# Performance work log

Hardware: AMD Instinct MI355X
Metric: run time of the kernel (lower is better)

Reference implementation:

```python
import jax, jax.numpy as jnp
import numpy as np

LMAX, MMAX = 4, 2
C_IN, C_OUT = 128, 128           # sphere_channels, m_output_channels
NUM_EXPERTS = 8
NUM_SYSTEMS = 16
NUM_EDGES = 12288
M_SIZE = [LMAX + 1, 2 * (LMAX - 1 + 1), 2 * (LMAX - 2 + 1)]  # [5, 8, 6]


def _mole_linear(x, W, ce, b=None):
    """MoLE linear: per-edge expert mixing of weights, equivalently mixing of
    per-expert outputs.  x: [N, in] or [N, 2, in]; W: [K, in, out]; ce: [N, K]."""
    if x.ndim == 2:
        z = jnp.einsum('ni,kio->nko', x, W)        # [N, K, out]
        y = jnp.einsum('nk,nko->no', ce, z)
    else:
        z = jnp.einsum('nci,kio->nkco', x, W)      # [N, K, 2, out]
        y = jnp.einsum('nk,nkco->nco', ce, z)
    if b is not None:
        y = y + ce @ b                              # mixed bias, b: [K, out]
    return y


def setup_inputs() -> dict:
    key = jax.random.key(0)
    ks = jax.random.split(key, 8)
    num_mcoef = sum(M_SIZE)  # 19
    x = jax.random.normal(ks[0], (NUM_EDGES, num_mcoef, C_IN), dtype=jnp.float32)
    x_edge = jax.random.normal(ks[1], (NUM_EDGES, C_IN), dtype=jnp.float32)
    expert_coefficients = jax.random.uniform(ks[2], (NUM_SYSTEMS, NUM_EXPERTS), dtype=jnp.float32)
    edge_batch = jax.random.randint(ks[3], (NUM_EDGES,), 0, NUM_SYSTEMS)
    # fc_m0: in = (lmax+1)*C, out = (lmax+1)*C_out, with bias
    in0 = (LMAX + 1) * C_IN
    out0 = (LMAX + 1) * C_OUT
    W_m0 = jax.random.normal(ks[4], (NUM_EXPERTS, in0, out0), dtype=jnp.float32) * 0.02
    b_m0 = jnp.zeros((NUM_EXPERTS, out0), dtype=jnp.float32)
    # so2_m_conv m: in = (lmax-m+1)*C, out = 2*(lmax-m+1)*C_out, no bias
    nc1 = LMAX - 1 + 1
    W_m1 = jax.random.normal(ks[5], (NUM_EXPERTS, nc1 * C_IN, 2 * nc1 * C_OUT), dtype=jnp.float32) * 0.02
    nc2 = LMAX - 2 + 1
    W_m2 = jax.random.normal(ks[6], (NUM_EXPERTS, nc2 * C_IN, 2 * nc2 * C_OUT), dtype=jnp.float32) * 0.02
    return {
        'x': x, 'x_edge': x_edge,
        'expert_coefficients': expert_coefficients, 'edge_batch': edge_batch,
        'W_m0': W_m0, 'b_m0': b_m0, 'W_m1': W_m1, 'W_m2': W_m2,
    }


def reference(x, x_edge, expert_coefficients, edge_batch, W_m0, b_m0, W_m1, W_m2):
    N = x.shape[0]
    ce = expert_coefficients[edge_batch]               # [N, K] per-edge mix coeffs
    x0, x1, x2 = jnp.split(x, np.cumsum(M_SIZE[:-1]), axis=1)
    # m = 0 branch (internal_weights=True -> no radial rescale)
    y0 = _mole_linear(x0.reshape(N, -1), W_m0, ce, b_m0)
    out = [y0.reshape(N, -1, C_OUT)]                   # [N, lmax+1, C_out]
    # m >= 1 branches: SO(2) real/imag recombination
    for m, Wm, xm in ((1, W_m1, x1), (2, W_m2, x2)):
        nc = LMAX - m + 1
        xm = xm.reshape(N, 2, nc * C_IN)
        ym = _mole_linear(xm, Wm, ce)                  # [N, 2, 2*nc*C_out]
        ym = ym.reshape(N, 4, nc * C_OUT)
        x_m_r = ym[:, 0] - ym[:, 3]                    # x_r_0 - x_i_1
        x_m_i = ym[:, 2] + ym[:, 1]                    # x_r_1 + x_i_0
        out.append(x_m_r.reshape(N, nc, C_OUT))
        out.append(x_m_i.reshape(N, nc, C_OUT))
    return jnp.concatenate(out, axis=1)                # [N, 19, C_out]
```

## Files before the change

### kernel.cpp

```cpp
#include <hip/hip_runtime.h>
#include <cstdint>

#define N_EDGES 12288
#define ROWLEN  2432
#define CAP     2048

typedef __bf16 bf16;
typedef __bf16 bf16x8 __attribute__((ext_vector_type(8)));
typedef __bf16 bf16x4 __attribute__((ext_vector_type(4)));
typedef float  f32x4  __attribute__((ext_vector_type(4)));

#define SYS0 (640*640   + 2048)
#define SYS1 (1024*1024 + 2048)
#define SYS2 (768*768   + 2048)

#define WS_IDX_OFF   1024
#define WS_BIAS_OFF  (WS_IDX_OFF + 16*CAP*4)
#define WS_W_OFF     (WS_BIAS_OFF + 16*640*4)

template<int B> struct Cfg;
template<> struct Cfg<0> { static constexpr int K=640,  KS=640, XOFF=0,    NT=5;
                           static constexpr size_t SYS=SYS0, WOFF=0; };
template<> struct Cfg<1> { static constexpr int K=1024, KS=512, XOFF=640,  NT=8;
                           static constexpr size_t SYS=SYS1, WOFF=(size_t)16*SYS0; };
template<> struct Cfg<2> { static constexpr int K=768,  KS=384, XOFF=1664, NT=6;
                           static constexpr size_t SYS=SYS2,
                           WOFF=(size_t)16*SYS0+(size_t)16*SYS1; };

__device__ __forceinline__ void async_copy16(const void* g, void* l) {
  auto gp = reinterpret_cast<const __attribute__((address_space(1))) unsigned int*>(
      reinterpret_cast<uintptr_t>(g));
  auto lp = reinterpret_cast<__attribute__((address_space(3))) unsigned int*>(
      (unsigned int)reinterpret_cast<uintptr_t>(l));
  __builtin_amdgcn_global_load_lds(gp, lp, 16, 0, 0);
}

template<int B>
__device__ __forceinline__ void mix_body(const float* __restrict__ Wsrc,
                                         const float* ce_s,
                                         unsigned short* __restrict__ Wz,
                                         int pos, int estart) {
  constexpr int N = Cfg<B>::K, KS = Cfg<B>::KS, NT = N / 128, HALF = N / 2;
  constexpr int SRC_STRIDE = KS * N;
  constexpr size_t DST_STRIDE = Cfg<B>::SYS;
  int nn = pos & 127, kgrp = (pos >> 7) & 3, rest = pos >> 9;
  int nt = rest % NT, kblk = rest / NT;
  int i0 = kblk * 32 + kgrp * 8;
  int c  = nt * 128 + nn;
  int si = i0, sc = c; float sg = 1.f;
  if (B > 0 && i0 >= KS) {
    si = i0 - KS;
    if (c < HALF) { sc = c + HALF; sg = -1.f; } else { sc = c - HALF; }
  }
  unsigned short* db = Wz + Cfg<B>::WOFF + (size_t)pos * 8;
  const float* p0 = Wsrc + (size_t)si * N + sc;
#pragma unroll 1
  for (int jh = 0; jh < 2; ++jh) {
    float w[8][4];
#pragma unroll
    for (int t = 0; t < 8; ++t) {
      int ee = (t + estart) & 7;
      const float* p = p0 + (size_t)ee * SRC_STRIDE + (size_t)(jh * 4) * N;
#pragma unroll
      for (int j = 0; j < 4; ++j) w[t][j] = sg * p[(size_t)j * N];
    }
#pragma unroll
    for (int s = 0; s < 16; ++s) {
      float a[4] = {0, 0, 0, 0};
#pragma unroll
      for (int t = 0; t < 8; ++t) {
        float cc = ce_s[s * 8 + ((t + estart) & 7)];
#pragma unroll
        for (int j = 0; j < 4; ++j) a[j] += cc * w[t][j];
      }
      bf16x4 v;
      v[0] = (bf16)a[0]; v[1] = (bf16)a[1]; v[2] = (bf16)a[2]; v[3] = (bf16)a[3];
      *(bf16x4*)(db + s * DST_STRIDE + jh * 4) = v;
    }
  }
}

__global__ __launch_bounds__(256) void prep_all(
    const float* __restrict__ W0, const float* __restrict__ W1,
    const float* __restrict__ W2, const float* __restrict__ ce,
    unsigned short* __restrict__ Wz,
    const int* __restrict__ eb, int* __restrict__ counts, int* __restrict__ idxb,
    const float* __restrict__ b0, float* __restrict__ bias) {
  __shared__ float ce_s[128];
  __shared__ int hcnt[16], hbase[16];
  int tid = threadIdx.x;
  int bx = blockIdx.x;
  if (bx < 1000) {
    if (tid < 128) ce_s[tid] = ce[tid];
    __syncthreads();
    int estart = bx & 7;
    if (bx < 200)      mix_body<0>(W0, ce_s, Wz, bx * 256 + tid, estart);
    else if (bx < 712) mix_body<1>(W1, ce_s, Wz, (bx - 200) * 256 + tid, estart);
    else               mix_body<2>(W2, ce_s, Wz, (bx - 712) * 256 + tid, estart);
  } else if (bx < 1048) {
    int t = (bx - 1000) * 256 + tid;
    if (tid < 16) hcnt[tid] = 0;
    __syncthreads();
    int s = -1, lp = 0;
    if (t < N_EDGES) { s = eb[t]; lp = atomicAdd(&hcnt[s], 1); }
    __syncthreads();
    if (tid < 16) hbase[tid] = atomicAdd(counts + tid * 16, hcnt[tid]);
    __syncthreads();
    if (s >= 0) { int p = hbase[s] + lp; if (p < CAP) idxb[s * CAP + p] = t; }
  } else {
    int t = (bx - 1048) * 256 + tid;
    int s = t / 640, c = t - s * 640;
    float a = 0.f;
#pragma unroll
    for (int e = 0; e < 8; ++e) a += ce[s * 8 + e] * b0[e * 640 + c];
    bias[t] = a;
  }
}

template<int B>
__device__ __forceinline__ void gemm_body(
    const float* __restrict__ x,
    const unsigned short* __restrict__ Wz,
    const int* __restrict__ counts, const int* __restrict__ idxb,
    const float* __restrict__ bias, float* __restrict__ out,
    int s, int mt, int nt2, char* sm, int* eidx)
{
  constexpr int K = Cfg<B>::K, NT = Cfg<B>::NT, KB = K / 32, XOFF = Cfg<B>::XOFF;
  int cnt = counts[s * 16];
  int m0 = mt * 128;
  if (m0 >= cnt) return;
  int tid = threadIdx.x;
  if (tid < 128) eidx[tid] = (m0 + tid < cnt) ? idxb[s * CAP + m0 + tid] : -1;
  __syncthreads();
  char* Acur = sm;          char* Anxt = sm + 8192;
  char* Bc = sm + 16384;    char* Bm = sm + 32768;    char* Bn = sm + 49152;
  int wv = tid >> 6, ln = tid & 63;
  int wm = wv >> 2, wn = wv & 3;
  int kq = ln >> 4, lm = ln & 15;
  int c0 = nt2 * 2;
  int c16 = tid & 7, rbase = tid >> 3;
  int kq_w = c16 >> 1, half = c16 & 1;
  const char* xb = (const char*)x;
  unsigned int aoff[2], kinc[2];
#pragma unroll
  for (int i = 0; i < 2; ++i) {
    int e = eidx[rbase + 64 * i];
    aoff[i] = (e >= 0) ? (unsigned int)(((size_t)e * ROWLEN + XOFF) * 4) : 0u;
    kinc[i] = (e >= 0) ? 128u : 0u;
  }
  const unsigned short* wb = Wz + Cfg<B>::WOFF + (size_t)s * Cfg<B>::SYS;

  f32x4 sreg[2];
  auto loadA = [&](int kb) __attribute__((always_inline)) {
#pragma unroll
    for (int i = 0; i < 2; ++i)
      sreg[i] = *(const f32x4*)(xb + aoff[i] + kb * kinc[i] + c16 * 16);
  };
  auto writeA = [&](char* dst) __attribute__((always_inline)) {
#pragma unroll
    for (int i = 0; i < 2; ++i) {
      int r = rbase + 64 * i;
      bf16x4 v;
      v[0] = (bf16)sreg[i][0]; v[1] = (bf16)sreg[i][1];
      v[2] = (bf16)sreg[i][2]; v[3] = (bf16)sreg[i][3];
      *(bf16x4*)(dst + kq_w * 2048 + ((r ^ (kq_w << 1)) * 16) + half * 8) = v;
    }
  };
  auto stageB = [&](int kb, char* dst) __attribute__((always_inline)) {
    const unsigned short* base = wb + (size_t)kb * (NT * 4096);
#pragma unroll
    for (int i = 0; i < 2; ++i) {
      int c = i * 512 + tid;
      int ck = c0 + (c >> 9); if (ck > NT - 1) ck = NT - 1;
      async_copy16(base + (size_t)ck * 4096 + (c & 511) * 8,
                   dst + (i * 512 + wv * 64) * 16);
    }
  };

  f32x4 acc[4][4];
#pragma unroll
  for (int i = 0; i < 4; ++i)
#pragma unroll
    for (int j = 0; j < 4; ++j) {
      acc[i][j][0] = 0.f; acc[i][j][1] = 0.f; acc[i][j][2] = 0.f; acc[i][j][3] = 0.f;
    }

  stageB(0, Bc);
  loadA(0);
  writeA(Acur);
  stageB(1, Bm);
  loadA(1);
  asm volatile("s_waitcnt lgkmcnt(0)" ::: "memory");
  __builtin_amdgcn_s_barrier();
  __builtin_amdgcn_sched_barrier(0);

#pragma unroll 1
  for (int kb = 0; kb < KB; ++kb) {
    if (kb + 2 < KB) stageB(kb + 2, Bn);
    __builtin_amdgcn_sched_barrier(0);
    bf16x8 af[4], bq[4];
#pragma unroll
    for (int mi = 0; mi < 4; ++mi) {
      int r = wm * 64 + mi * 16 + lm;
      af[mi] = *(const bf16x8*)(Acur + kq * 2048 + ((r ^ (kq << 1)) * 16));
    }
#pragma unroll
    for (int ni = 0; ni < 4; ++ni)
      bq[ni] = *(const bf16x8*)(Bc + (wn >> 1) * 8192 + kq * 2048 +
                                (((wn & 1) * 64 + ni * 16 + lm) * 16));
    __builtin_amdgcn_s_setprio(1);
#pragma unroll
    for (int mi = 0; mi < 4; ++mi)
#pragma unroll
      for (int ni = 0; ni < 4; ++ni)
        acc[mi][ni] = __builtin_amdgcn_mfma_f32_16x16x32_bf16(af[mi], bq[ni], acc[mi][ni], 0, 0, 0);
    __builtin_amdgcn_s_setprio(0);
    if (kb + 1 < KB) {
      writeA(Anxt);
      if (kb + 2 < KB) loadA(kb + 2);
    }
    asm volatile("s_waitcnt lgkmcnt(0)" ::: "memory");
    __builtin_amdgcn_s_barrier();
    __builtin_amdgcn_sched_barrier(0);
    { char* t = Acur; Acur = Anxt; Anxt = t; }
    { char* tb = Bc; Bc = Bm; Bm = Bn; Bn = tb; }
  }
  int cc = c0 + (wn >> 1);
  if (cc >= NT) return;
  int colb = cc * 128 + (wn & 1) * 64;
  float bv[4] = {0, 0, 0, 0};
  if (B == 0) {
#pragma unroll
    for (int ni = 0; ni < 4; ++ni)
      bv[ni] = bias[s * 640 + colb + ni * 16 + lm];
  }
#pragma unroll
  for (int mi = 0; mi < 4; ++mi) {
#pragma unroll
    for (int r = 0; r < 4; ++r) {
      int row = wm * 64 + mi * 16 + kq * 4 + r;
      int e = eidx[row];
      if (e < 0) continue;
      float* po = out + (size_t)e * ROWLEN + XOFF + colb + lm;
#pragma unroll
      for (int ni = 0; ni < 4; ++ni) po[ni * 16] = acc[mi][ni][r] + bv[ni];
    }
  }
}

__global__ __launch_bounds__(512, 4) void gemm_all(
    const float* __restrict__ x,
    const unsigned short* __restrict__ Wz,
    const int* __restrict__ counts, const int* __restrict__ idxb,
    const float* __restrict__ bias, float* __restrict__ out) {
  extern __shared__ char sm[];
  __shared__ int eidx[128];
  int g = blockIdx.x;
  int xcd = g & 7, j = g >> 3;
  int s = xcd + 8 * (j / 160);
  int r = j % 160;
  int mt = r / 10, bx = r % 10;
  if (bx < 3)      gemm_body<0>(x, Wz, counts, idxb, bias, out, s, mt, bx,     sm, eidx);
  else if (bx < 7) gemm_body<1>(x, Wz, counts, idxb, bias, out, s, mt, bx - 3, sm, eidx);
  else             gemm_body<2>(x, Wz, counts, idxb, bias, out, s, mt, bx - 7, sm, eidx);
}

extern "C" void kernel_launch(void* const* d_in, const int* in_sizes, int n_in,
                              void* d_out, int out_size, void* d_ws, size_t ws_size,
                              hipStream_t stream) {
  const float* x  = (const float*)d_in[0];
  const float* ce = (const float*)d_in[2];
  const int*   eb = (const int*)d_in[3];
  const float* W0 = (const float*)d_in[4];
  const float* b0 = (const float*)d_in[5];
  const float* W1 = (const float*)d_in[6];
  const float* W2 = (const float*)d_in[7];
  float* out = (float*)d_out;
  char* ws = (char*)d_ws;
  int*   counts = (int*)ws;
  int*   idxb   = (int*)(ws + WS_IDX_OFF);
  float* bias   = (float*)(ws + WS_BIAS_OFF);
  unsigned short* Wz = (unsigned short*)(ws + WS_W_OFF);

  hipMemsetAsync(ws, 0, 1024, stream);
  prep_all<<<1088, 256, 0, stream>>>(W0, W1, W2, ce, Wz, eb, counts, idxb, b0, bias);
  gemm_all<<<2560, 512, 65536, stream>>>(x, Wz, counts, idxb, bias, out);
}
```

Measured before the change: 336.5 us.

## Fuse prep and GEMM kernels with per-branch flag-based dependency waits

Merges the weight-mixing, bucketing and bias prep kernel into the GEMM kernel. The first 256 blocks do the prep work and signal per-branch counters with release atomics, and GEMM blocks spin on their branch's counter before starting. This removes a kernel launch boundary and lets GEMM for branches whose weights are ready overlap the remaining prep. In exchange it relies on the prep blocks being scheduled before the spinning blocks, and the spin-waits cost occupancy.

Measured after the change: 650.9 us. 93.4% more time.

```diff
diff --git a/kernel.cpp b/kernel.cpp
--- a/kernel.cpp
+++ b/kernel.cpp
@@ -14,9 +14,14 @@
 #define SYS1 (1024*1024 + 2048)
 #define SYS2 (768*768   + 2048)
 
-#define WS_IDX_OFF   1024
+#define WS_FLAG_OFF  1024
+#define WS_IDX_OFF   2048
 #define WS_BIAS_OFF  (WS_IDX_OFF + 16*CAP*4)
 #define WS_W_OFF     (WS_BIAS_OFF + 16*640*4)
+
+#define MIXP0  51200
+#define MIXP01 182272
+#define MIXP   256000
 
 template<int B> struct Cfg;
 template<> struct Cfg<0> { static constexpr int K=640,  KS=640, XOFF=0,    NT=5;
@@ -77,43 +82,6 @@
       v[0] = (bf16)a[0]; v[1] = (bf16)a[1]; v[2] = (bf16)a[2]; v[3] = (bf16)a[3];
       *(bf16x4*)(db + s * DST_STRIDE + jh * 4) = v;
     }
-  }
-}
-
-__global__ __launch_bounds__(256) void prep_all(
-    const float* __restrict__ W0, const float* __restrict__ W1,
-    const float* __restrict__ W2, const float* __restrict__ ce,
-    unsigned short* __restrict__ Wz,
-    const int* __restrict__ eb, int* __restrict__ counts, int* __restrict__ idxb,
-    const float* __restrict__ b0, float* __restrict__ bias) {
-  __shared__ float ce_s[128];
-  __shared__ int hcnt[16], hbase[16];
-  int tid = threadIdx.x;
-  int bx = blockIdx.x;
-  if (bx < 1000) {
-    if (tid < 128) ce_s[tid] = ce[tid];
-    __syncthreads();
-    int estart = bx & 7;
-    if (bx < 200)      mix_body<0>(W0, ce_s, Wz, bx * 256 + tid, estart);
-    else if (bx < 712) mix_body<1>(W1, ce_s, Wz, (bx - 200) * 256 + tid, estart);
-    else               mix_body<2>(W2, ce_s, Wz, (bx - 712) * 256 + tid, estart);
-  } else if (bx < 1048) {
-    int t = (bx - 1000) * 256 + tid;
-    if (tid < 16) hcnt[tid] = 0;
-    __syncthreads();
-    int s = -1, lp = 0;
-    if (t < N_EDGES) { s = eb[t]; lp = atomicAdd(&hcnt[s], 1); }
-    __syncthreads();
-    if (tid < 16) hbase[tid] = atomicAdd(counts + tid * 16, hcnt[tid]);
-    __syncthreads();
-    if (s >= 0) { int p = hbase[s] + lp; if (p < CAP) idxb[s * CAP + p] = t; }
-  } else {
-    int t = (bx - 1048) * 256 + tid;
-    int s = t / 640, c = t - s * 640;
-    float a = 0.f;
-#pragma unroll
-    for (int e = 0; e < 8; ++e) a += ce[s * 8 + e] * b0[e * 640 + c];
-    bias[t] = a;
   }
 }
 
@@ -248,18 +216,85 @@
   }
 }
 
-__global__ __launch_bounds__(512, 4) void gemm_all(
+__global__ __launch_bounds__(512, 4) void fused_all(
     const float* __restrict__ x,
-    const unsigned short* __restrict__ Wz,
-    const int* __restrict__ counts, const int* __restrict__ idxb,
-    const float* __restrict__ bias, float* __restrict__ out) {
+    const float* __restrict__ W0, const float* __restrict__ W1,
+    const float* __restrict__ W2, const float* __restrict__ ce,
+    const int* __restrict__ eb, const float* __restrict__ b0,
+    unsigned short* __restrict__ Wz, int* __restrict__ counts,
+    int* __restrict__ idxb, float* __restrict__ bias,
+    int* __restrict__ flags, float* __restrict__ out) {
   extern __shared__ char sm[];
   __shared__ int eidx[128];
+  __shared__ float ce_s[128];
+  __shared__ int hcnt[16], hbase[16];
+  int tid = threadIdx.x;
   int g = blockIdx.x;
+
+  if (g < 256) {
+    if (tid < 128) ce_s[tid] = ce[tid];
+    if (g < 24) {
+      if (tid < 16) hcnt[tid] = 0;
+      __syncthreads();
+      int t = g * 512 + tid;
+      int s0 = eb[t];
+      int p0 = atomicAdd(&hcnt[s0], 1);
+      __syncthreads();
+      if (tid < 16) hbase[tid] = atomicAdd(counts + tid * 16, hcnt[tid]);
+      __syncthreads();
+      int q0 = hbase[s0] + p0;
+      if (q0 < CAP) idxb[s0 * CAP + q0] = t;
+    } else if (g < 44) {
+      int t = (g - 24) * 512 + tid;
+      int si = t / 640, c = t - si * 640;
+      float a = 0.f;
+#pragma unroll
+      for (int e = 0; e < 8; ++e) a += ce[si * 8 + e] * b0[e * 640 + c];
+      bias[t] = a;
+    }
+    __syncthreads();
+    if (g < 44) {
+      __threadfence();
+      if (tid == 0) {
+        __hip_atomic_fetch_add(flags + 0, 1, __ATOMIC_RELEASE, __HIP_MEMORY_SCOPE_AGENT);
+        __hip_atomic_fetch_add(flags + 1, 1, __ATOMIC_RELEASE, __HIP_MEMORY_SCOPE_AGENT);
+        __hip_atomic_fetch_add(flags + 2, 1, __ATOMIC_RELEASE, __HIP_MEMORY_SCOPE_AGENT);
+      }
+    }
+    int lo = g * 1000, estart = g & 7;
+#pragma unroll 1
+    for (int q = 0; q < 2; ++q) {
+      if (q == 1 && tid >= 488) break;
+      int idx = lo + q * 512 + tid;
+      if (idx < MIXP0)       mix_body<0>(W0, ce_s, Wz, idx, estart);
+      else if (idx < MIXP01) mix_body<1>(W1, ce_s, Wz, idx - MIXP0, estart);
+      else                   mix_body<2>(W2, ce_s, Wz, idx - MIXP01, estart);
+    }
+    __syncthreads();
+    __threadfence();
+    if (tid == 0) {
+      int hi = lo + 1000;
+      if (lo < MIXP0)
+        __hip_atomic_fetch_add(flags + 0, 1, __ATOMIC_RELEASE, __HIP_MEMORY_SCOPE_AGENT);
+      if (hi > MIXP0 && lo < MIXP01)
+        __hip_atomic_fetch_add(flags + 1, 1, __ATOMIC_RELEASE, __HIP_MEMORY_SCOPE_AGENT);
+      if (hi > MIXP01)
+        __hip_atomic_fetch_add(flags + 2, 1, __ATOMIC_RELEASE, __HIP_MEMORY_SCOPE_AGENT);
+    }
+  }
+
   int xcd = g & 7, j = g >> 3;
   int s = xcd + 8 * (j / 160);
   int r = j % 160;
   int mt = r / 10, bx = r % 10;
+  int br = (bx < 3) ? 0 : (bx < 7) ? 1 : 2;
+  int tgt = (br == 0) ? 96 : (br == 1) ? 176 : 118;
+  if (tid == 0) {
+    while (__hip_atomic_load(flags + br, __ATOMIC_ACQUIRE, __HIP_MEMORY_SCOPE_AGENT) < tgt)
+      __builtin_amdgcn_s_sleep(32);
+  }
+  __syncthreads();
+
   if (bx < 3)      gemm_body<0>(x, Wz, counts, idxb, bias, out, s, mt, bx,     sm, eidx);
   else if (bx < 7) gemm_body<1>(x, Wz, counts, idxb, bias, out, s, mt, bx - 3, sm, eidx);
   else             gemm_body<2>(x, Wz, counts, idxb, bias, out, s, mt, bx - 7, sm, eidx);
@@ -278,11 +313,12 @@
   float* out = (float*)d_out;
   char* ws = (char*)d_ws;
   int*   counts = (int*)ws;
+  int*   flags  = (int*)(ws + WS_FLAG_OFF);
   int*   idxb   = (int*)(ws + WS_IDX_OFF);
   float* bias   = (float*)(ws + WS_BIAS_OFF);
   unsigned short* Wz = (unsigned short*)(ws + WS_W_OFF);
 
-  hipMemsetAsync(ws, 0, 1024, stream);
-  prep_all<<<1088, 256, 0, stream>>>(W0, W1, W2, ce, Wz, eb, counts, idxb, b0, bias);
-  gemm_all<<<2560, 512, 65536, stream>>>(x, Wz, counts, idxb, bias, out);
-}
+  hipMemsetAsync(ws, 0, 2048, stream);
+  fused_all<<<2560, 512, 65536, stream>>>(x, W0, W1, W2, ce, eb, b0,
+                                          Wz, counts, idxb, bias, flags, out);
+}
```
